# Optimization experiments

Measured on AMD Instinct MI355X. Metric: run time of the kernel, lower is better.

## Reference

```python
import jax, jax.numpy as jnp
import numpy as np

B, N, D, E, HEADS = 2, 256, 768, 8192, 8
HD = D // HEADS
EPS = 1e-5


def _lin(x, w, b):
    return x @ w.T + b


def setup_inputs() -> dict:
    key = jax.random.key(0)
    ks = iter(jax.random.split(key, 64))

    def W(*s):
        return jax.random.normal(next(ks), s, jnp.float32) * 0.02

    inp = {
        "node_embeddings": jax.random.normal(next(ks), (B, N, D), jnp.float32),
        "edge_weights": jax.random.uniform(next(ks), (E,), jnp.float32),
        "edge_indices": jax.random.randint(next(ks), (E, 2), 0, N, jnp.int32),
        # object classifier: D->D->D//2->8
        "oc_w1": W(D, D), "oc_b1": jnp.zeros((D,), jnp.float32),
        "oc_w2": W(D // 2, D), "oc_b2": jnp.zeros((D // 2,), jnp.float32),
        "oc_w3": W(8, D // 2), "oc_b3": jnp.zeros((8,), jnp.float32),
        # importance predictor: D->D//2->D//4->1
        "ip_w1": W(D // 2, D), "ip_b1": jnp.zeros((D // 2,), jnp.float32),
        "ip_w2": W(D // 4, D // 2), "ip_b2": jnp.zeros((D // 4,), jnp.float32),
        "ip_w3": W(1, D // 4), "ip_b3": jnp.zeros((1,), jnp.float32),
        # relation classifier: 2D->D->D//2->8
        "rc_w1": W(D, 2 * D), "rc_b1": jnp.zeros((D,), jnp.float32),
        "rc_w2": W(D // 2, D), "rc_b2": jnp.zeros((D // 2,), jnp.float32),
        "rc_w3": W(8, D // 2), "rc_b3": jnp.zeros((8,), jnp.float32),
        # attention in/out projections
        "attn_in_w": W(3 * D, D), "attn_in_b": jnp.zeros((3 * D,), jnp.float32),
        "attn_out_w": W(D, D), "attn_out_b": jnp.zeros((D,), jnp.float32),
    }
    for l in range(3):
        inp[f"gnn{l}_ws"] = W(D, D)
        inp[f"gnn{l}_bs"] = jnp.zeros((D,), jnp.float32)
        inp[f"gnn{l}_wn"] = W(D, D)
        inp[f"gnn{l}_bn"] = jnp.zeros((D,), jnp.float32)
        inp[f"gnn{l}_g"] = jnp.ones((D,), jnp.float32)
        inp[f"gnn{l}_beta"] = jnp.zeros((D,), jnp.float32)
    return inp


def reference(node_embeddings, edge_weights, edge_indices,
              oc_w1, oc_b1, oc_w2, oc_b2, oc_w3, oc_b3,
              ip_w1, ip_b1, ip_w2, ip_b2, ip_w3, ip_b3,
              rc_w1, rc_b1, rc_w2, rc_b2, rc_w3, rc_b3,
              attn_in_w, attn_in_b, attn_out_w, attn_out_b,
              gnn0_ws, gnn0_bs, gnn0_wn, gnn0_bn, gnn0_g, gnn0_beta,
              gnn1_ws, gnn1_bs, gnn1_wn, gnn1_bn, gnn1_g, gnn1_beta,
              gnn2_ws, gnn2_bs, gnn2_wn, gnn2_bn, gnn2_g, gnn2_beta):
    x = node_embeddings  # [B,N,D]
    src, tgt = edge_indices[:, 0], edge_indices[:, 1]

    # object classifier (dropout is identity in eval)
    h = jax.nn.relu(_lin(x, oc_w1, oc_b1))
    h = jax.nn.relu(_lin(h, oc_w2, oc_b2))
    object_cls = jax.nn.softmax(_lin(h, oc_w3, oc_b3), axis=-1)

    # importance predictor
    h = jax.nn.relu(_lin(x, ip_w1, ip_b1))
    h = jax.nn.relu(_lin(h, ip_w2, ip_b2))
    importance = jax.nn.sigmoid(_lin(h, ip_w3, ip_b3))

    # 3 GNN layers: self-linear + weighted scatter-add neighbor aggregation
    g = x
    layers = [(gnn0_ws, gnn0_bs, gnn0_wn, gnn0_bn, gnn0_g, gnn0_beta),
              (gnn1_ws, gnn1_bs, gnn1_wn, gnn1_bn, gnn1_g, gnn1_beta),
              (gnn2_ws, gnn2_bs, gnn2_wn, gnn2_bn, gnn2_g, gnn2_beta)]
    for ws, bs, wn, bn, gm, bt in layers:
        self_f = _lin(g, ws, bs)
        # vectorized scatter-add: agg[b,tgt] += w_e * g[b,src]
        agg = jnp.zeros_like(g).at[:, tgt, :].add(edge_weights[None, :, None] * g[:, src, :])
        neigh_f = _lin(agg, wn, bn)
        o = jax.nn.relu(self_f + neigh_f)
        mu = o.mean(axis=-1, keepdims=True)
        var = o.var(axis=-1, keepdims=True)  # biased, as torch LayerNorm
        g = gm * (o - mu) / jnp.sqrt(var + EPS) + bt

    # multi-head self-attention (torch MultiheadAttention, batch_first)
    qkv = _lin(g, attn_in_w, attn_in_b)  # [B,N,3D]
    q, k, v = jnp.split(qkv, 3, axis=-1)

    def heads(t):
        return t.reshape(B, N, HEADS, HD).transpose(0, 2, 1, 3)  # [B,H,N,hd]

    q, k, v = heads(q), heads(k), heads(v)
    scores = jnp.einsum('bhqd,bhkd->bhqk', q, k) / jnp.sqrt(jnp.float32(HD))
    attn = jax.nn.softmax(scores, axis=-1)
    ctx = jnp.einsum('bhqk,bhkd->bhqd', attn, v).transpose(0, 2, 1, 3).reshape(B, N, D)
    attended = _lin(ctx, attn_out_w, attn_out_b)  # [B,N,D]
    attn_weights = attn.mean(axis=1)  # torch averages heads -> [B,N,N]

    # all O(N^2) upper-triangular pairs, same (i<j) row-major order as the loop
    ii, jj = np.triu_indices(N, k=1)
    pair = jnp.concatenate([attended[:, ii, :], attended[:, jj, :]], axis=-1)  # [B,P,2D]
    h = jax.nn.relu(_lin(pair, rc_w1, rc_b1))
    h = jax.nn.relu(_lin(h, rc_w2, rc_b2))
    relation = jax.nn.softmax(_lin(h, rc_w3, rc_b3), axis=-1)  # [B,P,8]

    return (object_cls, relation, importance, attended, attn_weights)
```

## Files before the change

### kernel.cpp

```cpp
#include <hip/hip_runtime.h>
#include <hip/hip_bf16.h>

typedef __bf16 bf16;
typedef __bf16 bf16x4 __attribute__((ext_vector_type(4)));
typedef __bf16 bf16x8 __attribute__((ext_vector_type(8)));
typedef float  f32x4  __attribute__((ext_vector_type(4)));

#define NB 2
#define NN 256
#define DD 768
#define EE 8192
#define NPAIR 32640

__device__ inline float wred_sum(float v) {
#pragma unroll
  for (int o = 32; o > 0; o >>= 1) v += __shfl_down(v, o, 64);
  return v;
}

typedef const __attribute__((address_space(1))) void GASV;
typedef __attribute__((address_space(3))) void LASV;
__device__ __forceinline__ void async_cp16(const void* g, void* l) {
  __builtin_amdgcn_global_load_lds((GASV*)g, (LASV*)l, 16, 0, 0);
}

struct CJob { const float* s; bf16* d; int n; };
struct CJobs { CJob j[15]; };
__global__ __launch_bounds__(256) void preamble(
    CJobs jobs, const int* __restrict__ eidx, int* __restrict__ estart,
    int* __restrict__ bucket, int2* __restrict__ pairs)
{
  int by = blockIdx.y, t = threadIdx.x;
  if (by < 15) {
    const CJob jb = jobs.j[by];
    int nv = jb.n >> 2;
    for (int i = blockIdx.x * 256 + t; i < nv; i += gridDim.x * 256) {
      float4 v = ((const float4*)jb.s)[i];
      bf16x4 pk = { (bf16)v.x, (bf16)v.y, (bf16)v.z, (bf16)v.w };
      *(bf16x4*)(jb.d + 4 * i) = pk;
    }
  } else if (by == 15) {
    if (blockIdx.x != 0) return;
    __shared__ int tg[EE];
    __shared__ int cnt[256];
    __shared__ int sst[257];
    cnt[t] = 0;
    for (int e = t; e < EE; e += 256) tg[e] = eidx[2 * e + 1];
    __syncthreads();
    for (int e = t; e < EE; e += 256) atomicAdd(&cnt[tg[e]], 1);
    __syncthreads();
    if (t == 0) { int s = 0; for (int i = 0; i < 256; ++i) { sst[i] = s; s += cnt[i]; } sst[256] = s; }
    __syncthreads();
    estart[t] = sst[t];
    if (t == 0) estart[256] = sst[256];
    cnt[t] = sst[t];
    __syncthreads();
    for (int e = t; e < EE; e += 256) {
      int p = atomicAdd(&cnt[tg[e]], 1);
      bucket[p] = e;
    }
  } else {
#pragma unroll
    for (int u = 0; u < 2; ++u) {
      int i = blockIdx.x + u * 128;
      if (i < 255) {
        int off = i * 255 - (i * (i - 1)) / 2;
        for (int j = i + 1 + t; j < NN; j += 256)
          pairs[off + (j - i - 1)] = make_int2(i, j);
      }
    }
  }
}

__device__ __forceinline__ void lin_core(
    int m0, int n0, const bf16* __restrict__ X, const bf16* __restrict__ W,
    int ldw, int wofs, const float* __restrict__ bias, const float* __restrict__ addF,
    bf16* __restrict__ outB, float* __restrict__ outF, int N, int K, int act)
{
  int lane = threadIdx.x & 63, lr = lane & 15, lq = lane >> 4;
  const bf16* xrow = X + (size_t)(m0 + lr) * K;
  const bf16* wbase = W + (size_t)wofs;
  f32x4 acc[2] = {};
  for (int k = 0; k < K; k += 32) {
    bf16x8 a = *(const bf16x8*)(xrow + k + lq * 8);
    bf16x8 b0 = *(const bf16x8*)(wbase + (size_t)(n0 + lr) * ldw + k + lq * 8);
    bf16x8 b1 = *(const bf16x8*)(wbase + (size_t)(n0 + 16 + lr) * ldw + k + lq * 8);
    acc[0] = __builtin_amdgcn_mfma_f32_16x16x32_bf16(a, b0, acc[0], 0, 0, 0);
    acc[1] = __builtin_amdgcn_mfma_f32_16x16x32_bf16(a, b1, acc[1], 0, 0, 0);
  }
#pragma unroll
  for (int t = 0; t < 2; ++t) {
    int col = n0 + t * 16 + lr;
    float bv = bias ? bias[col] : 0.0f;
#pragma unroll
    for (int r = 0; r < 4; ++r) {
      int row = m0 + lq * 4 + r;
      size_t o = (size_t)row * N + col;
      float v = acc[t][r] + bv;
      if (addF) v += addF[o];
      if (act) v = fmaxf(v, 0.0f);
      if (outB) outB[o] = (bf16)v;
      if (outF) outF[o] = v;
    }
  }
}

__global__ __launch_bounds__(128) void linear_mfma(
    const bf16* __restrict__ X, const bf16* __restrict__ W, int ldw, int wofs,
    const float* __restrict__ bias, const float* __restrict__ addF,
    bf16* __restrict__ outB, float* __restrict__ outF,
    int N, int K, int act)
{
  int wave = threadIdx.x >> 6;
  lin_core((blockIdx.x * 2 + wave) * 16, blockIdx.y * 32,
           X, W, ldw, wofs, bias, addF, outB, outF, N, K, act);
}

struct LinJob {
  const bf16* X; const bf16* W; int ldw; int wofs;
  const float* bias; const float* addF; bf16* outB; float* outF;
  int N, K, act, gy;
};
__global__ __launch_bounds__(128) void linear_mfma2(LinJob j0, LinJob j1)
{
  LinJob j = blockIdx.z ? j1 : j0;
  if ((int)blockIdx.y >= j.gy) return;
  int wave = threadIdx.x >> 6;
  lin_core((blockIdx.x * 2 + wave) * 16, blockIdx.y * 32,
           j.X, j.W, j.ldw, j.wofs, j.bias, j.addF, j.outB, j.outF, j.N, j.K, j.act);
}

__global__ __launch_bounds__(256) void gnn_stage1(
    const bf16* __restrict__ g, const bf16* __restrict__ ws, const float* __restrict__ bs,
    float* __restrict__ selfF,
    const float* __restrict__ ew, const int* __restrict__ eidx,
    const int* __restrict__ estart, const int* __restrict__ bucket, bf16* __restrict__ agg)
{
  int bid = blockIdx.x, t = threadIdx.x;
  if (bid < 192) {
    int wave = t >> 6;
    lin_core(((bid & 7) * 4 + wave) * 16, (bid >> 3) * 32,
             g, ws, 768, 0, bs, nullptr, nullptr, selfF, 768, 768, 0);
    return;
  }
  __shared__ int   ssrc[256];
  __shared__ float sw[256];
  int e0 = bid - 192;
  int tgt = e0 & 255, b = e0 >> 8;
  int s = estart[tgt], e = estart[tgt + 1];
  s = max(0, min(s, EE));
  e = max(s, min(e, EE));
  const bf16* gb = g + (size_t)b * NN * DD;
  float a0 = 0, a1 = 0, a2 = 0, a3 = 0;
  for (int base = s; base < e; base += 256) {
    int nchunk = min(256, e - base);
    if (t < nchunk) {
      int eid = bucket[base + t];
      eid = max(0, min(eid, EE - 1));
      ssrc[t] = eidx[2 * eid] & (NN - 1);
      sw[t] = ew[eid];
    }
    __syncthreads();
    if (t < 192) {
      for (int q = 0; q < nchunk; ++q) {
        float w = sw[q];
        bf16x4 v = *(const bf16x4*)(gb + (size_t)ssrc[q] * DD + 4 * t);
        a0 += w * (float)v[0]; a1 += w * (float)v[1];
        a2 += w * (float)v[2]; a3 += w * (float)v[3];
      }
    }
    __syncthreads();
  }
  if (t < 192) {
    bf16x4 o = { (bf16)a0, (bf16)a1, (bf16)a2, (bf16)a3 };
    *(bf16x4*)(agg + ((size_t)b * NN + tgt) * DD + 4 * t) = o;
  }
}

__global__ __launch_bounds__(256) void layer_norm(
    const float* __restrict__ o, const float* __restrict__ gm,
    const float* __restrict__ bt, bf16* __restrict__ gout)
{
  __shared__ float red[8];
  int row = blockIdx.x, t = threadIdx.x;
  const float* orow = o + (size_t)row * DD;
  float v0 = orow[t], v1 = orow[t + 256], v2 = orow[t + 512];
  float s = v0 + v1 + v2;
  float q = v0 * v0 + v1 * v1 + v2 * v2;
  float ws_ = wred_sum(s), wq = wred_sum(q);
  if ((t & 63) == 0) { red[t >> 6] = ws_; red[4 + (t >> 6)] = wq; }
  __syncthreads();
  float S = red[0] + red[1] + red[2] + red[3];
  float Q = red[4] + red[5] + red[6] + red[7];
  float mu = S * (1.0f / 768.0f);
  float var = Q * (1.0f / 768.0f) - mu * mu;
  float rstd = rsqrtf(var + 1e-5f);
  bf16* gr = gout + (size_t)row * DD;
  gr[t]       = (bf16)(gm[t]       * (v0 - mu) * rstd + bt[t]);
  gr[t + 256] = (bf16)(gm[t + 256] * (v1 - mu) * rstd + bt[t + 256]);
  gr[t + 512] = (bf16)(gm[t + 512] * (v2 - mu) * rstd + bt[t + 512]);
}

__global__ __launch_bounds__(256) void attn_kernel(
    const bf16* __restrict__ qkv, float* __restrict__ aw, bf16* __restrict__ ctx)
{
  __shared__ float qs[96];
  __shared__ float ps[256];
  __shared__ float part[192];
  __shared__ float red[8];
  int qi = blockIdx.x, h = blockIdx.y, b = blockIdx.z, t = threadIdx.x;
  const bf16* qrow = qkv + ((size_t)(b * NN + qi)) * 2304 + h * 96;
  if (t < 96) qs[t] = (float)qrow[t];
  __syncthreads();
  const bf16* krow = qkv + ((size_t)(b * NN + t)) * 2304 + 768 + h * 96;
  float s = 0;
#pragma unroll
  for (int i = 0; i < 12; ++i) {
    bf16x8 kv = *(const bf16x8*)(krow + 8 * i);
#pragma unroll
    for (int j = 0; j < 8; ++j) s += qs[8 * i + j] * (float)kv[j];
  }
  s *= 0.10206207261596577f;
  float wm = s;
#pragma unroll
  for (int o = 32; o > 0; o >>= 1) wm = fmaxf(wm, __shfl_down(wm, o, 64));
  if ((t & 63) == 0) red[t >> 6] = wm;
  __syncthreads();
  float MX = fmaxf(fmaxf(red[0], red[1]), fmaxf(red[2], red[3]));
  float e = expf(s - MX);
  float wsum = wred_sum(e);
  if ((t & 63) == 0) red[4 + (t >> 6)] = wsum;
  __syncthreads();
  float SUM = red[4] + red[5] + red[6] + red[7];
  float p = e / SUM;
  ps[t] = p;
  atomicAdd(&aw[((size_t)(b * NN + qi)) * NN + t], p * 0.125f);
  __syncthreads();
  if (t < 192) {
    int d = t % 96, half = t / 96;
    const bf16* vbase = qkv + (size_t)b * NN * 2304 + 1536 + h * 96 + d;
    float a0 = 0, a1 = 0, a2 = 0, a3 = 0;
    int k0 = half * 128;
    for (int k = k0; k < k0 + 128; k += 4) {
      a0 += ps[k]     * (float)vbase[(size_t)k * 2304];
      a1 += ps[k + 1] * (float)vbase[(size_t)(k + 1) * 2304];
      a2 += ps[k + 2] * (float)vbase[(size_t)(k + 2) * 2304];
      a3 += ps[k + 3] * (float)vbase[(size_t)(k + 3) * 2304];
    }
    part[t] = (a0 + a1) + (a2 + a3);
  }
  __syncthreads();
  if (t < 96)
    ctx[((size_t)(b * NN + qi)) * DD + h * 96 + t] = (bf16)(part[t] + part[t + 96]);
}

__global__ __launch_bounds__(256) void small_heads(
    const bf16* __restrict__ hOC, const float* __restrict__ w3, const float* __restrict__ b3,
    float* __restrict__ outOC,
    const bf16* __restrict__ hIP, const float* __restrict__ w1, const float* __restrict__ b1,
    float* __restrict__ outIP)
{
  int t = threadIdx.x;
  int wave = t >> 6, lane = t & 63;
  if (blockIdx.x < 32) {
    __shared__ float sw3[8 * 384];
    for (int i = t; i < 8 * 384; i += 256) sw3[i] = w3[i];
    __syncthreads();
    int k0 = lane * 6;
#pragma unroll
    for (int i = 0; i < 4; ++i) {
      int r = blockIdx.x * 16 + wave * 4 + i;
      const bf16* hr = hOC + (size_t)r * 384;
      float hv[6];
#pragma unroll
      for (int j = 0; j < 6; ++j) hv[j] = (float)hr[k0 + j];
      float lg[8];
#pragma unroll
      for (int c = 0; c < 8; ++c) {
        float p = 0;
#pragma unroll
        for (int j = 0; j < 6; ++j) p += hv[j] * sw3[c * 384 + k0 + j];
        lg[c] = wred_sum(p);
      }
      if (lane == 0) {
        float mx = lg[0] + b3[0];
#pragma unroll
        for (int c = 0; c < 8; ++c) { lg[c] += b3[c]; mx = fmaxf(mx, lg[c]); }
        float ex[8], sum = 0;
#pragma unroll
        for (int c = 0; c < 8; ++c) { ex[c] = expf(lg[c] - mx); sum += ex[c]; }
        float inv = 1.0f / sum;
#pragma unroll
        for (int c = 0; c < 8; ++c) outOC[(size_t)r * 8 + c] = ex[c] * inv;
      }
    }
  } else {
    __shared__ float sw1[192];
    if (t < 192) sw1[t] = w1[t];
    __syncthreads();
    int k0 = lane * 3;
#pragma unroll
    for (int i = 0; i < 4; ++i) {
      int r = (blockIdx.x - 32) * 16 + wave * 4 + i;
      const bf16* hr = hIP + (size_t)r * 192;
      float p = (float)hr[k0] * sw1[k0] + (float)hr[k0 + 1] * sw1[k0 + 1]
              + (float)hr[k0 + 2] * sw1[k0 + 2];
      float s = wred_sum(p);
      if (lane == 0) outIP[r] = 1.0f / (1.0f + expf(-(s + b1[0])));
    }
  }
}

__global__ __launch_bounds__(256) void h2_gemm(
    const bf16* __restrict__ Af, const bf16* __restrict__ Bf,
    const bf16* __restrict__ w2, const float* __restrict__ b2,
    const float* __restrict__ w3, const int2* __restrict__ pairs,
    float* __restrict__ logP)
{
  __shared__ bf16x8 sh1[512];
  __shared__ bf16x8 sw2[768];
  __shared__ int rA[128], rB[128];
  int tid = threadIdx.x;
  int r0 = blockIdx.x * 128;
  int bb = (r0 >= NPAIR) ? 1 : 0;
  int n0 = blockIdx.y * 192;
  if (tid < 128) {
    int2 ij = pairs[r0 - bb * NPAIR + tid];
    rA[tid] = (bb * NN + ij.x) * DD;
    rB[tid] = (bb * NN + ij.y) * DD;
  }
  __syncthreads();
  int hrow = tid >> 1, hp = (tid & 1) * 2;
  const bf16* ar = Af + rA[hrow] + hp * 8;
  const bf16* br = Bf + rB[hrow] + hp * 8;
  int hslot = ((hrow >> 4) << 6) + (hp << 4) + (hrow & 15);
  int srow[3], spl[3];
#pragma unroll
  for (int q = 0; q < 3; ++q) {
    int a = q * 256 + tid;
    srow[q] = ((a >> 6) << 4) + (a & 15);
    spl[q] = (a >> 4) & 3;
  }
  int wave = tid >> 6, lane = tid & 63, lr = lane & 15, lq = lane >> 4;
  int wr = wave >> 1, wc = wave & 1;
  f32x4 acc[4][6] = {};
  for (int k0 = 0; k0 < 768; k0 += 32) {
#pragma unroll
    for (int q = 0; q < 3; ++q)
      async_cp16(w2 + (size_t)(n0 + srow[q]) * 768 + k0 + spl[q] * 8,
                 (char*)sw2 + (q * 256 + tid) * 16);
    bf16x8 a0 = *(const bf16x8*)(ar + k0);
    bf16x8 a1 = *(const bf16x8*)(ar + k0 + 8);
    bf16x8 b0 = *(const bf16x8*)(br + k0);
    bf16x8 b1 = *(const bf16x8*)(br + k0 + 8);
    bf16x8 h0, h1v;
#pragma unroll
    for (int j = 0; j < 8; ++j) {
      h0[j]  = (bf16)fmaxf((float)a0[j] + (float)b0[j], 0.f);
      h1v[j] = (bf16)fmaxf((float)a1[j] + (float)b1[j], 0.f);
    }
    sh1[hslot] = h0;
    sh1[hslot + 16] = h1v;
    __syncthreads();
    bf16x8 af[4], bfr[6];
#pragma unroll
    for (int rf = 0; rf < 4; ++rf)
      af[rf] = sh1[(wr * 4 + rf) * 64 + lq * 16 + lr];
#pragma unroll
    for (int cf = 0; cf < 6; ++cf)
      bfr[cf] = sw2[(wc * 6 + cf) * 64 + lq * 16 + lr];
#pragma unroll
    for (int rf = 0; rf < 4; ++rf)
#pragma unroll
      for (int cf = 0; cf < 6; ++cf)
        acc[rf][cf] = __builtin_amdgcn_mfma_f32_16x16x32_bf16(af[rf], bfr[cf], acc[rf][cf], 0, 0, 0);
    __syncthreads();
  }
  char* zone = (wave < 2) ? ((char*)sw2 + wave * 3328)
                          : ((char*)sh1 + (wave - 2) * 3328);
  bf16x8 w3f[3];
#pragma unroll
  for (int ks = 0; ks < 3; ++ks) {
    bf16x8 f = {};
    if (lr < 8) {
      const float* wsrc = w3 + lr * 384 + n0 + wc * 96 + ks * 32 + lq * 8;
#pragma unroll
      for (int j = 0; j < 8; ++j) f[j] = (bf16)wsrc[j];
    }
    w3f[ks] = f;
  }
  float* lp = logP + (size_t)((n0 >= 192 ? 2 : 0) + wc) * 65280 * 8;
  bf16* zb = (bf16*)zone;
#pragma unroll
  for (int rf = 0; rf < 4; ++rf) {
#pragma unroll
    for (int cf = 0; cf < 6; ++cf) {
      int col = n0 + wc * 96 + cf * 16 + lr;
      float bv2 = b2[col];
#pragma unroll
      for (int r = 0; r < 4; ++r)
        zb[(lq * 4 + r) * 104 + cf * 16 + lr] = (bf16)fmaxf(acc[rf][cf][r] + bv2, 0.f);
    }
    f32x4 lacc = {};
#pragma unroll
    for (int ks = 0; ks < 3; ++ks) {
      bf16x8 afr = *(const bf16x8*)(zone + lr * 208 + ks * 64 + lq * 16);
      lacc = __builtin_amdgcn_mfma_f32_16x16x32_bf16(afr, w3f[ks], lacc, 0, 0, 0);
    }
    if (lr < 8) {
#pragma unroll
      for (int r = 0; r < 4; ++r) {
        int grow = r0 + wr * 64 + rf * 16 + lq * 4 + r;
        lp[(size_t)grow * 8 + lr] = lacc[r];
      }
    }
  }
}

__global__ __launch_bounds__(256) void relsoftmax(
    const float* __restrict__ logP, const float* __restrict__ b3,
    float* __restrict__ out)
{
  int row = blockIdx.x * 256 + threadIdx.x;
  float lg[8];
#pragma unroll
  for (int c = 0; c < 8; ++c) lg[c] = b3[c];
#pragma unroll
  for (int p = 0; p < 4; ++p) {
    const float* lp = logP + ((size_t)p * 65280 + row) * 8;
#pragma unroll
    for (int c = 0; c < 8; ++c) lg[c] += lp[c];
  }
  float mx = lg[0];
#pragma unroll
  for (int c = 1; c < 8; ++c) mx = fmaxf(mx, lg[c]);
  float ex[8], sum = 0;
#pragma unroll
  for (int c = 0; c < 8; ++c) { ex[c] = expf(lg[c] - mx); sum += ex[c]; }
  float inv = 1.0f / sum;
#pragma unroll
  for (int c = 0; c < 8; ++c) out[(size_t)row * 8 + c] = ex[c] * inv;
}

extern "C" void kernel_launch(void* const* d_in, const int* in_sizes, int n_in,
                              void* d_out, int out_size, void* d_ws, size_t ws_size,
                              hipStream_t stream)
{
  (void)in_sizes; (void)n_in; (void)out_size; (void)ws_size;
  const float* x    = (const float*)d_in[0];
  const float* ew   = (const float*)d_in[1];
  const int*   eidx = (const int*)d_in[2];
  const float* oc_w1 = (const float*)d_in[3];  const float* oc_b1 = (const float*)d_in[4];
  const float* oc_w2 = (const float*)d_in[5];  const float* oc_b2 = (const float*)d_in[6];
  const float* oc_w3 = (const float*)d_in[7];  const float* oc_b3 = (const float*)d_in[8];
  const float* ip_w1 = (const float*)d_in[9];  const float* ip_b1 = (const float*)d_in[10];
  const float* ip_w2 = (const float*)d_in[11]; const float* ip_b2 = (const float*)d_in[12];
  const float* ip_w3 = (const float*)d_in[13]; const float* ip_b3 = (const float*)d_in[14];
  const float* rc_w1 = (const float*)d_in[15]; const float* rc_b1 = (const float*)d_in[16];
  const float* rc_w2 = (const float*)d_in[17]; const float* rc_b2 = (const float*)d_in[18];
  const float* rc_w3 = (const float*)d_in[19]; const float* rc_b3 = (const float*)d_in[20];
  const float* at_iw = (const float*)d_in[21]; const float* at_ib = (const float*)d_in[22];
  const float* at_ow = (const float*)d_in[23]; const float* at_ob = (const float*)d_in[24];

  float* out = (float*)d_out;
  float* out_oc  = out;
  float* out_rel = out + 4096;
  float* out_imp = out + 526336;
  float* out_att = out + 526848;
  float* out_aw  = out + 920064;

  char* wp = (char*)d_ws;
  auto alloc = [&](size_t bytes) { char* p = wp; wp += (bytes + 255) & ~(size_t)255; return p; };
  float* logP  = (float*)alloc((size_t)4 * 65280 * 8 * 4);
  float* selfF = (float*)alloc((size_t)512 * 768 * 4);
  float* oBuf  = (float*)alloc((size_t)512 * 768 * 4);
  bf16* AfB  = (bf16*)alloc((size_t)512 * 768 * 2);
  bf16* BfB  = (bf16*)alloc((size_t)512 * 768 * 2);
  bf16* xb   = (bf16*)alloc((size_t)512 * 768 * 2);
  bf16* g0   = (bf16*)alloc((size_t)512 * 768 * 2);
  bf16* g1   = (bf16*)alloc((size_t)512 * 768 * 2);
  bf16* hA   = (bf16*)alloc((size_t)512 * 768 * 2);
  bf16* hB   = (bf16*)alloc((size_t)512 * 384 * 2);
  bf16* hI1  = (bf16*)alloc((size_t)512 * 384 * 2);
  bf16* hI2  = (bf16*)alloc((size_t)512 * 192 * 2);
  bf16* aggB = (bf16*)alloc((size_t)512 * 768 * 2);
  bf16* qkv  = (bf16*)alloc((size_t)512 * 2304 * 2);
  bf16* ctx  = (bf16*)alloc((size_t)512 * 768 * 2);
  bf16* attB = (bf16*)alloc((size_t)512 * 768 * 2);
  bf16* w_oc1 = (bf16*)alloc((size_t)768 * 768 * 2);
  bf16* w_oc2 = (bf16*)alloc((size_t)384 * 768 * 2);
  bf16* w_ip1 = (bf16*)alloc((size_t)384 * 768 * 2);
  bf16* w_ip2 = (bf16*)alloc((size_t)192 * 384 * 2);
  bf16* w_rc1 = (bf16*)alloc((size_t)768 * 1536 * 2);
  bf16* w_rc2 = (bf16*)alloc((size_t)384 * 768 * 2);
  bf16* w_aiw = (bf16*)alloc((size_t)2304 * 768 * 2);
  bf16* w_aow = (bf16*)alloc((size_t)768 * 768 * 2);
  bf16* w_gnn[6];
  for (int i = 0; i < 6; ++i) w_gnn[i] = (bf16*)alloc((size_t)768 * 768 * 2);
  int2* pairs = (int2*)alloc((size_t)NPAIR * 8);
  int* estart = (int*)alloc(257 * 4);
  int* bucket = (int*)alloc((size_t)EE * 4);

  dim3 blk(256);
  dim3 blk128(128);

  CJobs cj;
  cj.j[0]  = { x,     xb,    512 * 768 };
  cj.j[1]  = { oc_w1, w_oc1, 768 * 768 };
  cj.j[2]  = { oc_w2, w_oc2, 384 * 768 };
  cj.j[3]  = { ip_w1, w_ip1, 384 * 768 };
  cj.j[4]  = { ip_w2, w_ip2, 192 * 384 };
  cj.j[5]  = { rc_w1, w_rc1, 768 * 1536 };
  cj.j[6]  = { rc_w2, w_rc2, 384 * 768 };
  cj.j[7]  = { at_iw, w_aiw, 2304 * 768 };
  cj.j[8]  = { at_ow, w_aow, 768 * 768 };
  for (int l = 0; l < 3; ++l) {
    cj.j[9 + 2 * l]  = { (const float*)d_in[25 + l * 6 + 0], w_gnn[2 * l],     768 * 768 };
    cj.j[10 + 2 * l] = { (const float*)d_in[25 + l * 6 + 2], w_gnn[2 * l + 1], 768 * 768 };
  }
  hipMemsetAsync(out_aw, 0, (size_t)NB * NN * NN * 4, stream);
  preamble<<<dim3(128, 17), blk, 0, stream>>>(cj, eidx, estart, bucket, pairs);

  {
    LinJob a = { xb, w_oc1, 768, 0, oc_b1, nullptr, hA,  nullptr, 768, 768, 1, 24 };
    LinJob b = { xb, w_ip1, 768, 0, ip_b1, nullptr, hI1, nullptr, 384, 768, 1, 12 };
    linear_mfma2<<<dim3(16, 24, 2), blk128, 0, stream>>>(a, b);
  }
  {
    LinJob a = { hA,  w_oc2, 768, 0, oc_b2, nullptr, hB,  nullptr, 384, 768, 1, 12 };
    LinJob b = { hI1, w_ip2, 384, 0, ip_b2, nullptr, hI2, nullptr, 192, 384, 1, 6 };
    linear_mfma2<<<dim3(16, 12, 2), blk128, 0, stream>>>(a, b);
  }
  small_heads<<<64, blk, 0, stream>>>(hB, oc_w3, oc_b3, out_oc, hI2, ip_w3, ip_b3, out_imp);

  const bf16* gcur = xb;
  bf16* gbufs[2] = { g0, g1 };
  for (int l = 0; l < 3; ++l) {
    const float* bs_ = (const float*)d_in[25 + l * 6 + 1];
    const float* bn_ = (const float*)d_in[25 + l * 6 + 3];
    const float* gm_ = (const float*)d_in[25 + l * 6 + 4];
    const float* bt_ = (const float*)d_in[25 + l * 6 + 5];
    gnn_stage1<<<704, blk, 0, stream>>>(gcur, w_gnn[2 * l], bs_, selfF, ew, eidx, estart, bucket, aggB);
    linear_mfma<<<dim3(16, 24), blk128, 0, stream>>>(aggB, w_gnn[2 * l + 1], 768, 0, bn_, selfF, nullptr, oBuf, 768, 768, 1);
    layer_norm<<<512, blk, 0, stream>>>(oBuf, gm_, bt_, gbufs[l & 1]);
    gcur = gbufs[l & 1];
  }

  linear_mfma<<<dim3(16, 72), blk128, 0, stream>>>(gcur, w_aiw, 768, 0, at_ib, nullptr, qkv, nullptr, 2304, 768, 0);
  attn_kernel<<<dim3(256, 8, 2), blk, 0, stream>>>(qkv, out_aw, ctx);
  linear_mfma<<<dim3(16, 24), blk128, 0, stream>>>(ctx, w_aow, 768, 0, at_ob, nullptr, attB, out_att, 768, 768, 0);

  {
    LinJob a = { attB, w_rc1, 1536, 0,   rc_b1,  nullptr, AfB, nullptr, 768, 768, 0, 24 };
    LinJob b = { attB, w_rc1, 1536, 768, nullptr, nullptr, BfB, nullptr, 768, 768, 0, 24 };
    linear_mfma2<<<dim3(16, 24, 2), blk128, 0, stream>>>(a, b);
  }
  h2_gemm<<<dim3(510, 2), blk, 0, stream>>>(AfB, BfB, w_rc2, rc_b2, rc_w3, pairs, logP);
  relsoftmax<<<255, blk, 0, stream>>>(logP, rc_b3, out_rel);
}
```

Before: 460.3 us.

## Fuse first GNN layer with classifier heads into merged launches; fold memset into preamble

Merges the first GNN layer's stages with the object-classifier and importance MLP layers into three combined kernels (mega1/mega2/mega3), so independent work shares each launch and fewer launches are issued. The attention-weight zeroing moves from a separate memset into an extra grid row of the preamble. The relation-classifier intermediate A/B buffers become fp32 instead of bf16, so the pair MLP reads twice the bytes but avoids one rounding step.

```diff
diff --git a/kernel.cpp b/kernel.cpp
--- a/kernel.cpp
+++ b/kernel.cpp
@@ -5,6 +5,7 @@
 typedef __bf16 bf16x4 __attribute__((ext_vector_type(4)));
 typedef __bf16 bf16x8 __attribute__((ext_vector_type(8)));
 typedef float  f32x4  __attribute__((ext_vector_type(4)));
+typedef float  f32x8  __attribute__((ext_vector_type(8)));
 
 #define NB 2
 #define NN 256
@@ -28,7 +29,7 @@
 struct CJobs { CJob j[15]; };
 __global__ __launch_bounds__(256) void preamble(
     CJobs jobs, const int* __restrict__ eidx, int* __restrict__ estart,
-    int* __restrict__ bucket, int2* __restrict__ pairs)
+    int* __restrict__ bucket, int2* __restrict__ pairs, float* __restrict__ aw)
 {
   int by = blockIdx.y, t = threadIdx.x;
   if (by < 15) {
@@ -59,7 +60,7 @@
       int p = atomicAdd(&cnt[tg[e]], 1);
       bucket[p] = e;
     }
-  } else {
+  } else if (by == 16) {
 #pragma unroll
     for (int u = 0; u < 2; ++u) {
       int i = blockIdx.x + u * 128;
@@ -69,6 +70,9 @@
           pairs[off + (j - i - 1)] = make_int2(i, j);
       }
     }
+  } else {
+    int idx = blockIdx.x * 256 + t;
+    ((float4*)aw)[idx] = make_float4(0.f, 0.f, 0.f, 0.f);
   }
 }
 
@@ -105,6 +109,16 @@
   }
 }
 
+__device__ __forceinline__ void lin256(
+    int bid, const bf16* X, const bf16* W, int ldw, int wofs,
+    const float* bias, const float* addF, bf16* outB, float* outF,
+    int N, int K, int act)
+{
+  int wave = threadIdx.x >> 6;
+  lin_core(((bid & 7) * 4 + wave) * 16, (bid >> 3) * 32,
+           X, W, ldw, wofs, bias, addF, outB, outF, N, K, act);
+}
+
 __global__ __launch_bounds__(128) void linear_mfma(
     const bf16* __restrict__ X, const bf16* __restrict__ W, int ldw, int wofs,
     const float* __restrict__ bias, const float* __restrict__ addF,
@@ -130,21 +144,18 @@
            j.X, j.W, j.ldw, j.wofs, j.bias, j.addF, j.outB, j.outF, j.N, j.K, j.act);
 }
 
-__global__ __launch_bounds__(256) void gnn_stage1(
-    const bf16* __restrict__ g, const bf16* __restrict__ ws, const float* __restrict__ bs,
-    float* __restrict__ selfF,
+__device__ __forceinline__ void gnn_s1_body(
+    int bid, const bf16* __restrict__ g, const bf16* __restrict__ ws,
+    const float* __restrict__ bs, float* __restrict__ selfF,
     const float* __restrict__ ew, const int* __restrict__ eidx,
-    const int* __restrict__ estart, const int* __restrict__ bucket, bf16* __restrict__ agg)
-{
-  int bid = blockIdx.x, t = threadIdx.x;
+    const int* __restrict__ estart, const int* __restrict__ bucket,
+    bf16* __restrict__ agg, int* ssrc, float* sw)
+{
+  int t = threadIdx.x;
   if (bid < 192) {
-    int wave = t >> 6;
-    lin_core(((bid & 7) * 4 + wave) * 16, (bid >> 3) * 32,
-             g, ws, 768, 0, bs, nullptr, nullptr, selfF, 768, 768, 0);
+    lin256(bid, g, ws, 768, 0, bs, nullptr, nullptr, selfF, 768, 768, 0);
     return;
   }
-  __shared__ int   ssrc[256];
-  __shared__ float sw[256];
   int e0 = bid - 192;
   int tgt = e0 & 255, b = e0 >> 8;
   int s = estart[tgt], e = estart[tgt + 1];
@@ -177,12 +188,58 @@
   }
 }
 
-__global__ __launch_bounds__(256) void layer_norm(
-    const float* __restrict__ o, const float* __restrict__ gm,
-    const float* __restrict__ bt, bf16* __restrict__ gout)
-{
-  __shared__ float red[8];
-  int row = blockIdx.x, t = threadIdx.x;
+__global__ __launch_bounds__(256) void gnn_stage1(
+    const bf16* __restrict__ g, const bf16* __restrict__ ws, const float* __restrict__ bs,
+    float* __restrict__ selfF,
+    const float* __restrict__ ew, const int* __restrict__ eidx,
+    const int* __restrict__ estart, const int* __restrict__ bucket, bf16* __restrict__ agg)
+{
+  __shared__ int   ssrc[256];
+  __shared__ float sw[256];
+  gnn_s1_body(blockIdx.x, g, ws, bs, selfF, ew, eidx, estart, bucket, agg, ssrc, sw);
+}
+
+__global__ __launch_bounds__(256) void mega1(
+    const bf16* __restrict__ xb, const bf16* __restrict__ ws0, const float* __restrict__ bs0,
+    float* __restrict__ selfF,
+    const float* __restrict__ ew, const int* __restrict__ eidx,
+    const int* __restrict__ estart, const int* __restrict__ bucket, bf16* __restrict__ agg,
+    const bf16* __restrict__ w_oc1, const float* __restrict__ oc_b1, bf16* __restrict__ hA,
+    const bf16* __restrict__ w_ip1, const float* __restrict__ ip_b1, bf16* __restrict__ hI1)
+{
+  __shared__ int   ssrc[256];
+  __shared__ float sw[256];
+  int bid = blockIdx.x;
+  if (bid < 704)
+    gnn_s1_body(bid, xb, ws0, bs0, selfF, ew, eidx, estart, bucket, agg, ssrc, sw);
+  else if (bid < 896)
+    lin256(bid - 704, xb, w_oc1, 768, 0, oc_b1, nullptr, hA, nullptr, 768, 768, 1);
+  else
+    lin256(bid - 896, xb, w_ip1, 768, 0, ip_b1, nullptr, hI1, nullptr, 384, 768, 1);
+}
+
+__global__ __launch_bounds__(256) void mega2(
+    const bf16* __restrict__ aggB, const bf16* __restrict__ wn0, const float* __restrict__ bn0,
+    const float* __restrict__ selfF, float* __restrict__ oBuf,
+    const bf16* __restrict__ hA, const bf16* __restrict__ w_oc2, const float* __restrict__ oc_b2,
+    bf16* __restrict__ hB,
+    const bf16* __restrict__ hI1, const bf16* __restrict__ w_ip2, const float* __restrict__ ip_b2,
+    bf16* __restrict__ hI2)
+{
+  int bid = blockIdx.x;
+  if (bid < 192)
+    lin256(bid, aggB, wn0, 768, 0, bn0, selfF, nullptr, oBuf, 768, 768, 1);
+  else if (bid < 288)
+    lin256(bid - 192, hA, w_oc2, 768, 0, oc_b2, nullptr, hB, nullptr, 384, 768, 1);
+  else
+    lin256(bid - 288, hI1, w_ip2, 384, 0, ip_b2, nullptr, hI2, nullptr, 192, 384, 1);
+}
+
+__device__ __forceinline__ void ln_body(
+    int row, const float* __restrict__ o, const float* __restrict__ gm,
+    const float* __restrict__ bt, bf16* __restrict__ gout, float* red)
+{
+  int t = threadIdx.x;
   const float* orow = o + (size_t)row * DD;
   float v0 = orow[t], v1 = orow[t + 256], v2 = orow[t + 512];
   float s = v0 + v1 + v2;
@@ -199,6 +256,74 @@
   gr[t]       = (bf16)(gm[t]       * (v0 - mu) * rstd + bt[t]);
   gr[t + 256] = (bf16)(gm[t + 256] * (v1 - mu) * rstd + bt[t + 256]);
   gr[t + 512] = (bf16)(gm[t + 512] * (v2 - mu) * rstd + bt[t + 512]);
+}
+
+__global__ __launch_bounds__(256) void layer_norm(
+    const float* __restrict__ o, const float* __restrict__ gm,
+    const float* __restrict__ bt, bf16* __restrict__ gout)
+{
+  __shared__ float red[8];
+  ln_body(blockIdx.x, o, gm, bt, gout, red);
+}
+
+__global__ __launch_bounds__(256) void mega3(
+    const float* __restrict__ oBuf, const float* __restrict__ gm0,
+    const float* __restrict__ bt0, bf16* __restrict__ gout,
+    const bf16* __restrict__ hOC, const float* __restrict__ w3, const float* __restrict__ b3,
+    float* __restrict__ outOC,
+    const bf16* __restrict__ hIP, const float* __restrict__ w1, const float* __restrict__ b1,
+    float* __restrict__ outIP)
+{
+  __shared__ float sh[3072];
+  int bid = blockIdx.x, t = threadIdx.x;
+  int wave = t >> 6, lane = t & 63;
+  if (bid < 512) {
+    ln_body(bid, oBuf, gm0, bt0, gout, sh);
+  } else if (bid < 544) {
+    for (int i = t; i < 8 * 384; i += 256) sh[i] = w3[i];
+    __syncthreads();
+    int k0 = lane * 6;
+#pragma unroll
+    for (int i = 0; i < 4; ++i) {
+      int r = (bid - 512) * 16 + wave * 4 + i;
+      const bf16* hr = hOC + (size_t)r * 384;
+      float hv[6];
+#pragma unroll
+      for (int j = 0; j < 6; ++j) hv[j] = (float)hr[k0 + j];
+      float lg[8];
+#pragma unroll
+      for (int c = 0; c < 8; ++c) {
+        float p = 0;
+#pragma unroll
+        for (int j = 0; j < 6; ++j) p += hv[j] * sh[c * 384 + k0 + j];
+        lg[c] = wred_sum(p);
+      }
+      if (lane == 0) {
+        float mx = lg[0] + b3[0];
+#pragma unroll
+        for (int c = 0; c < 8; ++c) { lg[c] += b3[c]; mx = fmaxf(mx, lg[c]); }
+        float ex[8], sum = 0;
+#pragma unroll
+        for (int c = 0; c < 8; ++c) { ex[c] = expf(lg[c] - mx); sum += ex[c]; }
+        float inv = 1.0f / sum;
+#pragma unroll
+        for (int c = 0; c < 8; ++c) outOC[(size_t)r * 8 + c] = ex[c] * inv;
+      }
+    }
+  } else {
+    if (t < 192) sh[t] = w1[t];
+    __syncthreads();
+    int k0 = lane * 3;
+#pragma unroll
+    for (int i = 0; i < 4; ++i) {
+      int r = (bid - 544) * 16 + wave * 4 + i;
+      const bf16* hr = hIP + (size_t)r * 192;
+      float p = (float)hr[k0] * sh[k0] + (float)hr[k0 + 1] * sh[k0 + 1]
+              + (float)hr[k0 + 2] * sh[k0 + 2];
+      float s = wred_sum(p);
+      if (lane == 0) outIP[r] = 1.0f / (1.0f + expf(-(s + b1[0])));
+    }
+  }
 }
 
 __global__ __launch_bounds__(256) void attn_kernel(
@@ -254,65 +379,8 @@
     ctx[((size_t)(b * NN + qi)) * DD + h * 96 + t] = (bf16)(part[t] + part[t + 96]);
 }
 
-__global__ __launch_bounds__(256) void small_heads(
-    const bf16* __restrict__ hOC, const float* __restrict__ w3, const float* __restrict__ b3,
-    float* __restrict__ outOC,
-    const bf16* __restrict__ hIP, const float* __restrict__ w1, const float* __restrict__ b1,
-    float* __restrict__ outIP)
-{
-  int t = threadIdx.x;
-  int wave = t >> 6, lane = t & 63;
-  if (blockIdx.x < 32) {
-    __shared__ float sw3[8 * 384];
-    for (int i = t; i < 8 * 384; i += 256) sw3[i] = w3[i];
-    __syncthreads();
-    int k0 = lane * 6;
-#pragma unroll
-    for (int i = 0; i < 4; ++i) {
-      int r = blockIdx.x * 16 + wave * 4 + i;
-      const bf16* hr = hOC + (size_t)r * 384;
-      float hv[6];
-#pragma unroll
-      for (int j = 0; j < 6; ++j) hv[j] = (float)hr[k0 + j];
-      float lg[8];
-#pragma unroll
-      for (int c = 0; c < 8; ++c) {
-        float p = 0;
-#pragma unroll
-        for (int j = 0; j < 6; ++j) p += hv[j] * sw3[c * 384 + k0 + j];
-        lg[c] = wred_sum(p);
-      }
-      if (lane == 0) {
-        float mx = lg[0] + b3[0];
-#pragma unroll
-        for (int c = 0; c < 8; ++c) { lg[c] += b3[c]; mx = fmaxf(mx, lg[c]); }
-        float ex[8], sum = 0;
-#pragma unroll
-        for (int c = 0; c < 8; ++c) { ex[c] = expf(lg[c] - mx); sum += ex[c]; }
-        float inv = 1.0f / sum;
-#pragma unroll
-        for (int c = 0; c < 8; ++c) outOC[(size_t)r * 8 + c] = ex[c] * inv;
-      }
-    }
-  } else {
-    __shared__ float sw1[192];
-    if (t < 192) sw1[t] = w1[t];
-    __syncthreads();
-    int k0 = lane * 3;
-#pragma unroll
-    for (int i = 0; i < 4; ++i) {
-      int r = (blockIdx.x - 32) * 16 + wave * 4 + i;
-      const bf16* hr = hIP + (size_t)r * 192;
-      float p = (float)hr[k0] * sw1[k0] + (float)hr[k0 + 1] * sw1[k0 + 1]
-              + (float)hr[k0 + 2] * sw1[k0 + 2];
-      float s = wred_sum(p);
-      if (lane == 0) outIP[r] = 1.0f / (1.0f + expf(-(s + b1[0])));
-    }
-  }
-}
-
 __global__ __launch_bounds__(256) void h2_gemm(
-    const bf16* __restrict__ Af, const bf16* __restrict__ Bf,
+    const float* __restrict__ Af, const float* __restrict__ Bf,
     const bf16* __restrict__ w2, const float* __restrict__ b2,
     const float* __restrict__ w3, const int2* __restrict__ pairs,
     float* __restrict__ logP)
@@ -331,8 +399,8 @@
   }
   __syncthreads();
   int hrow = tid >> 1, hp = (tid & 1) * 2;
-  const bf16* ar = Af + rA[hrow] + hp * 8;
-  const bf16* br = Bf + rB[hrow] + hp * 8;
+  const float* ar = Af + rA[hrow] + hp * 8;
+  const float* br = Bf + rB[hrow] + hp * 8;
   int hslot = ((hrow >> 4) << 6) + (hp << 4) + (hrow & 15);
   int srow[3], spl[3];
 #pragma unroll
@@ -349,15 +417,15 @@
     for (int q = 0; q < 3; ++q)
       async_cp16(w2 + (size_t)(n0 + srow[q]) * 768 + k0 + spl[q] * 8,
                  (char*)sw2 + (q * 256 + tid) * 16);
-    bf16x8 a0 = *(const bf16x8*)(ar + k0);
-    bf16x8 a1 = *(const bf16x8*)(ar + k0 + 8);
-    bf16x8 b0 = *(const bf16x8*)(br + k0);
-    bf16x8 b1 = *(const bf16x8*)(br + k0 + 8);
+    f32x8 a0 = *(const f32x8*)(ar + k0);
+    f32x8 b0 = *(const f32x8*)(br + k0);
+    f32x8 a1 = *(const f32x8*)(ar + k0 + 8);
+    f32x8 b1 = *(const f32x8*)(br + k0 + 8);
     bf16x8 h0, h1v;
 #pragma unroll
     for (int j = 0; j < 8; ++j) {
-      h0[j]  = (bf16)fmaxf((float)a0[j] + (float)b0[j], 0.f);
-      h1v[j] = (bf16)fmaxf((float)a1[j] + (float)b1[j], 0.f);
+      h0[j]  = (bf16)fmaxf(a0[j] + b0[j], 0.f);
+      h1v[j] = (bf16)fmaxf(a1[j] + b1[j], 0.f);
     }
     sh1[hslot] = h0;
     sh1[hslot + 16] = h1v;
@@ -474,8 +542,8 @@
   float* logP  = (float*)alloc((size_t)4 * 65280 * 8 * 4);
   float* selfF = (float*)alloc((size_t)512 * 768 * 4);
   float* oBuf  = (float*)alloc((size_t)512 * 768 * 4);
-  bf16* AfB  = (bf16*)alloc((size_t)512 * 768 * 2);
-  bf16* BfB  = (bf16*)alloc((size_t)512 * 768 * 2);
+  float* Af    = (float*)alloc((size_t)512 * 768 * 4);
+  float* Bf    = (float*)alloc((size_t)512 * 768 * 4);
   bf16* xb   = (bf16*)alloc((size_t)512 * 768 * 2);
   bf16* g0   = (bf16*)alloc((size_t)512 * 768 * 2);
   bf16* g1   = (bf16*)alloc((size_t)512 * 768 * 2);
@@ -518,24 +586,23 @@
     cj.j[9 + 2 * l]  = { (const float*)d_in[25 + l * 6 + 0], w_gnn[2 * l],     768 * 768 };
     cj.j[10 + 2 * l] = { (const float*)d_in[25 + l * 6 + 2], w_gnn[2 * l + 1], 768 * 768 };
   }
-  hipMemsetAsync(out_aw, 0, (size_t)NB * NN * NN * 4, stream);
-  preamble<<<dim3(128, 17), blk, 0, stream>>>(cj, eidx, estart, bucket, pairs);
-
-  {
-    LinJob a = { xb, w_oc1, 768, 0, oc_b1, nullptr, hA,  nullptr, 768, 768, 1, 24 };
-    LinJob b = { xb, w_ip1, 768, 0, ip_b1, nullptr, hI1, nullptr, 384, 768, 1, 12 };
-    linear_mfma2<<<dim3(16, 24, 2), blk128, 0, stream>>>(a, b);
-  }
-  {
-    LinJob a = { hA,  w_oc2, 768, 0, oc_b2, nullptr, hB,  nullptr, 384, 768, 1, 12 };
-    LinJob b = { hI1, w_ip2, 384, 0, ip_b2, nullptr, hI2, nullptr, 192, 384, 1, 6 };
-    linear_mfma2<<<dim3(16, 12, 2), blk128, 0, stream>>>(a, b);
-  }
-  small_heads<<<64, blk, 0, stream>>>(hB, oc_w3, oc_b3, out_oc, hI2, ip_w3, ip_b3, out_imp);
-
-  const bf16* gcur = xb;
-  bf16* gbufs[2] = { g0, g1 };
-  for (int l = 0; l < 3; ++l) {
+  preamble<<<dim3(128, 18), blk, 0, stream>>>(cj, eidx, estart, bucket, pairs, out_aw);
+
+  const float* bs0 = (const float*)d_in[26];
+  const float* bn0 = (const float*)d_in[28];
+  const float* gm0 = (const float*)d_in[29];
+  const float* bt0 = (const float*)d_in[30];
+
+  mega1<<<992, blk, 0, stream>>>(xb, w_gnn[0], bs0, selfF, ew, eidx, estart, bucket, aggB,
+                                 w_oc1, oc_b1, hA, w_ip1, ip_b1, hI1);
+  mega2<<<336, blk, 0, stream>>>(aggB, w_gnn[1], bn0, selfF, oBuf,
+                                 hA, w_oc2, oc_b2, hB, hI1, w_ip2, ip_b2, hI2);
+  mega3<<<576, blk, 0, stream>>>(oBuf, gm0, bt0, g0,
+                                 hB, oc_w3, oc_b3, out_oc, hI2, ip_w3, ip_b3, out_imp);
+
+  const bf16* gcur = g0;
+  bf16* gbufs[2] = { g1, g0 };
+  for (int l = 1; l < 3; ++l) {
     const float* bs_ = (const float*)d_in[25 + l * 6 + 1];
     const float* bn_ = (const float*)d_in[25 + l * 6 + 3];
     const float* gm_ = (const float*)d_in[25 + l * 6 + 4];
@@ -551,10 +618,10 @@
   linear_mfma<<<dim3(16, 24), blk128, 0, stream>>>(ctx, w_aow, 768, 0, at_ob, nullptr, attB, out_att, 768, 768, 0);
 
   {
-    LinJob a = { attB, w_rc1, 1536, 0,   rc_b1,  nullptr, AfB, nullptr, 768, 768, 0, 24 };
-    LinJob b = { attB, w_rc1, 1536, 768, nullptr, nullptr, BfB, nullptr, 768, 768, 0, 24 };
+    LinJob a = { attB, w_rc1, 1536, 0,   rc_b1,  nullptr, nullptr, Af, 768, 768, 0, 24 };
+    LinJob b = { attB, w_rc1, 1536, 768, nullptr, nullptr, nullptr, Bf, 768, 768, 0, 24 };
     linear_mfma2<<<dim3(16, 24, 2), blk128, 0, stream>>>(a, b);
   }
-  h2_gemm<<<dim3(510, 2), blk, 0, stream>>>(AfB, BfB, w_rc2, rc_b2, rc_w3, pairs, logP);
+  h2_gemm<<<dim3(510, 2), blk, 0, stream>>>(Af, Bf, w_rc2, rc_b2, rc_w3, pairs, logP);
   relsoftmax<<<255, blk, 0, stream>>>(logP, rc_b3, out_rel);
 }
```

Result: no change. 459.7 us (-0.1%).
